# Optimization experiments

Measured on AMD Instinct MI355X. Metric: run time of the kernel, lower is better.

Reference implementation:

```python
import jax, jax.numpy as jnp
import numpy as np

TOP_K = 2          # routed top_k = top_k - num_shared_experts = 3 - 1
CAP_FACTOR = 1.1   # capacity_factor


def setup_inputs() -> dict:
    key = jax.random.key(0)
    ks = jax.random.split(key, 12)
    B, S, D, E = 4, 2048, 1024, 7
    s = 0.02
    return {
        "x": jax.random.normal(ks[0], (B, S, D), jnp.float32),
        "noise": jax.random.normal(ks[1], (B, S, E), jnp.float32),
        "Wr": jax.random.normal(ks[2], (D, E)) * s, "br": jnp.zeros((E,)),
        "Wn": jax.random.normal(ks[3], (D, E)) * s, "bn": jnp.zeros((E,)),
        "W1": jax.random.normal(ks[4], (E, D, D)) * s, "b1": jnp.zeros((E, D)),
        "W2": jax.random.normal(ks[5], (E, D, D)) * s, "b2": jnp.zeros((E, D)),
        "Ws1": jax.random.normal(ks[6], (D, D)) * s, "bs1": jnp.zeros((D,)),
        "Ws2": jax.random.normal(ks[7], (D, D)) * s, "bs2": jnp.zeros((D,)),
    }


def reference(x, noise, Wr, br, Wn, bn, W1, b1, W2, b2, Ws1, bs1, Ws2, bs2):
    B, S, D = x.shape
    E = Wr.shape[1]
    N = B * S
    C = int(N * TOP_K / E * CAP_FACTOR)  # per-expert capacity (static)

    # shared expert (Dropout inactive at inference)
    x_shared = jax.nn.relu(x @ Ws1 + bs1) @ Ws2 + bs2

    # --- noisy top-k router ---
    logits = x @ Wr + br
    noisy = logits + noise * jax.nn.softplus(x @ Wn + bn)
    vals, idx = jax.lax.top_k(noisy, TOP_K)                    # [B,S,K]
    onehot = jax.nn.one_hot(idx, E, dtype=x.dtype)             # [B,S,K,E]
    probs_k = jax.nn.softmax(vals, axis=-1)                    # softmax over -inf-masked logits == softmax over top-k vals
    router_probs = jnp.einsum('bske,bsk->bse', onehot, probs_k)
    expert_mask = onehot.sum(-2)
    lbl = E * (router_probs.mean((0, 1)) * expert_mask.mean((0, 1))).sum()

    # --- capacity-limited dispatch, first-come-first-served in flat token order ---
    flat_x = x.reshape(N, D)
    flat_g = router_probs.reshape(N, E)
    m = (expert_mask.reshape(N, E) > 0).T                      # [E,N] token->expert assignment
    pos = jnp.cumsum(m.astype(jnp.int32), axis=1) - 1          # slot within expert
    valid = m & (pos < C)
    token = jnp.arange(N, dtype=jnp.int32)
    dest = jnp.where(valid, jnp.arange(E, dtype=jnp.int32)[:, None] * C + pos, E * C)
    idxs = jnp.full((E * C + 1,), N, dtype=jnp.int32)
    idxs = idxs.at[dest.reshape(-1)].set(jnp.broadcast_to(token, (E, N)).reshape(-1))
    idxs = idxs[:E * C].reshape(E, C)                          # token id per slot, N = padding

    xpad = jnp.concatenate([flat_x, jnp.zeros((1, D), x.dtype)], axis=0)
    gpad = jnp.concatenate([flat_g, jnp.zeros((1, E), x.dtype)], axis=0)
    xe = xpad[idxs]                                            # [E,C,D]
    h = jax.nn.relu(jnp.einsum('ecd,edh->ech', xe, W1) + b1[:, None, :])
    out = jnp.einsum('ech,ehd->ecd', h, W2) + b2[:, None, :]
    g = (gpad[idxs] * jnp.eye(E, dtype=x.dtype)[:, None, :]).sum(-1)  # [E,C] gate per slot
    slot_valid = (idxs < N).astype(x.dtype)
    weighted = out * (g * slot_valid)[..., None]

    upd = jnp.zeros((N + 1, D), x.dtype).at[idxs.reshape(-1)].add(weighted.reshape(-1, D))[:N]
    final = upd.reshape(B, S, D) + x_shared
    return final, lbl
```

## Files before the change

kernel.cpp:

```cpp
#include <hip/hip_runtime.h>
#include <math.h>

typedef unsigned short u16;
typedef __attribute__((ext_vector_type(4))) float f32x4;
typedef __bf16 bf16x8 __attribute__((ext_vector_type(8)));

#define NTOK 8192
#define DDIM 1024
#define NEXP 7
#define CAPC 2574
#define CPAD 2688
#define EBLK 1176
#define TBLK 1688
#define XCHK 211

__device__ inline float bf2f(u16 u) {
    union { unsigned int i; float f; } c; c.i = ((unsigned int)u) << 16; return c.f;
}
__device__ inline u16 f2bf(float f) {
    union { float f; unsigned int i; } c; c.f = f;
    unsigned int u = c.i;
    unsigned int r = (u + 0x7fffu + ((u >> 16) & 1u)) >> 16;
    return (u16)r;
}

__device__ inline void gl2lds16(const u16* g, const u16* l) {
    __builtin_amdgcn_global_load_lds(
        (const __attribute__((address_space(1))) unsigned int*)g,
        (__attribute__((address_space(3))) unsigned int*)l, 16, 0, 0);
}

__global__ void k_zero(float* out, long n) {
    long i = (long)blockIdx.x * 256 + threadIdx.x;
    long stride = (long)gridDim.x * 256;
    for (; i < n; i += stride) out[i] = 0.f;
}

__device__ inline void tile_transpose(const float* __restrict__ src, u16* __restrict__ dst,
                                      int k0, int n0, int tid, u16 (*tbuf)[256]) {
#pragma unroll
    for (int p = 0; p < 16; ++p) {
        int kl = p * 16 + (tid >> 4);
        int nl = (tid & 15) * 4;
        float4 v = *(const float4*)(src + (long)(k0 + kl) * 1024 + n0 + nl);
        int s = (tid & 7) << 3;
        int kx = kl ^ s;
        tbuf[nl + 0][kx] = f2bf(v.x);
        tbuf[nl + 1][kx] = f2bf(v.y);
        tbuf[nl + 2][kx] = f2bf(v.z);
        tbuf[nl + 3][kx] = f2bf(v.w);
    }
    __syncthreads();
#pragma unroll
    for (int q = 0; q < 8; ++q) {
        int nl = q * 8 + (tid >> 5);
        int kl = (tid & 31) * 8;
        int s = ((nl >> 2) & 7) << 3;
        const u16* pr = &tbuf[nl][kl ^ s];
        ushort4 a = *(const ushort4*)pr;
        ushort4 b = *(const ushort4*)(pr + 4);
        u16* pd = dst + (long)(n0 + nl) * 1024 + k0 + kl;
        *(ushort4*)pd = a;
        *(ushort4*)(pd + 4) = b;
    }
}

__global__ void k_prep(const float* __restrict__ x, u16* __restrict__ xb,
                       int* __restrict__ slot_token, u16* __restrict__ zrow,
                       const float* __restrict__ W1, const float* __restrict__ Ws1,
                       u16* __restrict__ Wt, u16* __restrict__ Wst,
                       const float* __restrict__ W2, const float* __restrict__ Ws2,
                       u16* __restrict__ Wt2, u16* __restrict__ Wst2) {
    __shared__ u16 tbuf[64][256];
    int bid = blockIdx.x, tid = threadIdx.x;
    if (bid < 4096) {
        int gid = bid * 256 + tid;
        int i = gid * 8;
        float4 a = *(const float4*)(x + i);
        float4 b = *(const float4*)(x + i + 4);
        ushort4 o0; o0.x = f2bf(a.x); o0.y = f2bf(a.y); o0.z = f2bf(a.z); o0.w = f2bf(a.w);
        ushort4 o1; o1.x = f2bf(b.x); o1.y = f2bf(b.y); o1.z = f2bf(b.z); o1.w = f2bf(b.w);
        *(ushort4*)(xb + i) = o0;
        *(ushort4*)(xb + i + 4) = o1;
        if (gid < DDIM) zrow[gid] = 0;
        if (gid < NEXP * CPAD) slot_token[gid] = NTOK;
        return;
    }
    int tb = bid - 4096;
    int set = tb >> 9;
    int t9 = tb & 511;
    int z = t9 >> 6;
    int rem = t9 & 63;
    int k0 = (rem >> 4) * 256;
    int n0 = (rem & 15) * 64;
    const float* srcE = set ? W2 : W1;
    const float* srcS = set ? Ws2 : Ws1;
    u16* dE = set ? Wt2 : Wt;
    u16* dS = set ? Wst2 : Wst;
    const float* src; u16* dst;
    if (z < 7) { src = srcE + (long)z * 1048576; dst = dE + (long)z * 1048576; }
    else       { src = srcS;                     dst = dS; }
    tile_transpose(src, dst, k0, n0, tid, tbuf);
}

__global__ void k_transpose(const float* __restrict__ srcE, const float* __restrict__ srcS,
                            u16* __restrict__ Wt, u16* __restrict__ Wst) {
    __shared__ u16 tbuf[64][256];
    int bid = blockIdx.x, tid = threadIdx.x;
    int z = bid >> 6;
    int rem = bid & 63;
    int k0 = (rem >> 4) * 256;
    int n0 = (rem & 15) * 64;
    const float* src; u16* dst;
    if (z < 7) { src = srcE + (long)z * 1048576; dst = Wt + (long)z * 1048576; }
    else       { src = srcS;                     dst = Wst; }
    tile_transpose(src, dst, k0, n0, tid, tbuf);
}

__global__ __launch_bounds__(512) void k_router(
    const float* __restrict__ x,
    const float* __restrict__ Wr, const float* __restrict__ Wn,
    double* __restrict__ arO, double* __restrict__ anO) {
    __shared__ float swr[7168];
    __shared__ float swn[7168];
    int tid = threadIdx.x;
    for (int i = tid; i < 7168; i += 512) { swr[i] = Wr[i]; swn[i] = Wn[i]; }
    __syncthreads();
    int lane = tid & 63, wv = tid >> 6;
    int t = blockIdx.x * 8 + wv;
    double ar[7] = {0,0,0,0,0,0,0}, an[7] = {0,0,0,0,0,0,0};
    for (int j = 0; j < 16; ++j) {
        int d = j * 64 + lane;
        double xd = (double)x[t * 1024 + d];
#pragma unroll
        for (int e = 0; e < 7; ++e) {
            ar[e] += xd * (double)swr[d * 7 + e];
            an[e] += xd * (double)swn[d * 7 + e];
        }
    }
#pragma unroll
    for (int e = 0; e < 7; ++e) {
        for (int o = 32; o > 0; o >>= 1) {
            ar[e] += __shfl_xor(ar[e], o);
            an[e] += __shfl_xor(an[e], o);
        }
    }
    if (lane == 0) {
#pragma unroll
        for (int e = 0; e < 7; ++e) { arO[t * 7 + e] = ar[e]; anO[t * 7 + e] = an[e]; }
    }
}

__global__ void k_tail(const double* __restrict__ arO, const double* __restrict__ anO,
                       const float* __restrict__ noise,
                       const float* __restrict__ br, const float* __restrict__ bn,
                       int* __restrict__ idx0, int* __restrict__ idx1,
                       float* __restrict__ p0, float* __restrict__ p1,
                       int* __restrict__ cntA, double* __restrict__ sumA) {
    int t = blockIdx.x * 256 + threadIdx.x;
    int lane = threadIdx.x & 63;
    double best = -1e300, second = -1e300; int b0 = 0, b1 = 0;
#pragma unroll
    for (int e = 0; e < 7; ++e) {
        double lg = arO[t * 7 + e] + (double)br[e];
        double z  = anO[t * 7 + e] + (double)bn[e];
        double sp = (z > 30.0) ? (z + log1p(exp(-z))) : log1p(exp(z));
        double v  = lg + (double)noise[t * 7 + e] * sp;
        if (v > best)        { second = best; b1 = b0; best = v; b0 = e; }
        else if (v > second) { second = v; b1 = e; }
    }
    double ex = exp(second - best);
    float q0 = (float)(1.0 / (1.0 + ex));
    float q1 = (float)(ex / (1.0 + ex));
    idx0[t] = b0; idx1[t] = b1; p0[t] = q0; p1[t] = q1;
    int chunk = t >> 6;
    double dq0 = (double)q0, dq1 = (double)q1;
#pragma unroll
    for (int e = 0; e < 7; ++e) {
        unsigned long long m = __ballot((b0 == e) || (b1 == e));
        double q = (b0 == e ? dq0 : 0.0) + (b1 == e ? dq1 : 0.0);
        for (int o = 32; o > 0; o >>= 1) q += __shfl_xor(q, o);
        if (lane == 0) { cntA[e * 128 + chunk] = __popcll(m); sumA[e * 128 + chunk] = q; }
    }
}

__global__ void k_scanbase(const int* __restrict__ cntA, const double* __restrict__ sumA,
                           int* __restrict__ baseA, int* __restrict__ cnt,
                           float* __restrict__ out) {
    __shared__ int s[7][128];
    __shared__ double rd[7][128];
    __shared__ int rawc[7];
    __shared__ double ps[7];
    int tid = threadIdx.x;
    int e = tid >> 7, i = tid & 127;
    int v = cntA[e * 128 + i];
    s[e][i] = v;
    rd[e][i] = sumA[e * 128 + i];
    __syncthreads();
    for (int o = 1; o < 128; o <<= 1) {
        int add = (i >= o) ? s[e][i - o] : 0;
        __syncthreads();
        s[e][i] += add;
        __syncthreads();
    }
    baseA[e * 128 + i] = s[e][i] - v;
    if (i == 127) { rawc[e] = s[e][127]; cnt[e] = (s[e][127] < CAPC) ? s[e][127] : CAPC; }
    for (int o = 64; o > 0; o >>= 1) {
        if (i < o) rd[e][i] += rd[e][i + o];
        __syncthreads();
    }
    if (i == 0) ps[e] = rd[e][0];
    __syncthreads();
    if (tid == 0) {
        double acc = 0.0;
        for (int ee = 0; ee < 7; ++ee) acc += ps[ee] * (double)rawc[ee];
        out[(long)NTOK * DDIM] = (float)(7.0 * acc / (8192.0 * 8192.0));
    }
}

__global__ void k_assign(const int* __restrict__ idx0, const int* __restrict__ idx1,
                         const int* __restrict__ baseA, int* __restrict__ slot_token,
                         int* __restrict__ ts0, int* __restrict__ ts1) {
    int lane = threadIdx.x & 63;
    int chunk = (blockIdx.x * 256 + threadIdx.x) >> 6;
    int t = chunk * 64 + lane;
    int i0 = idx0[t], i1 = idx1[t];
    int myts0 = -1, myts1 = -1;
    unsigned long long lt = (1ull << lane) - 1ull;
#pragma unroll
    for (int e = 0; e < 7; ++e) {
        bool has = (i0 == e) || (i1 == e);
        unsigned long long m = __ballot(has);
        int pre = __popcll(m & lt);
        int pos = baseA[e * 128 + chunk] + pre;
        if (has && pos < CAPC) {
            int slot = e * CPAD + pos;
            slot_token[slot] = t;
            if (i0 == e) myts0 = slot; else myts1 = slot;
        }
    }
    ts0[t] = myts0; ts1[t] = myts1;
}

template <bool GATHER, bool MODE_H>
__global__ __launch_bounds__(256) void k_gemm(
    const u16* __restrict__ AbaseE, const u16* __restrict__ AbaseS,
    const int* __restrict__ gidx, const u16* __restrict__ zrow,
    const u16* __restrict__ WtE, const u16* __restrict__ WtS,
    const float* __restrict__ biasE, const float* __restrict__ biasS,
    u16* __restrict__ outE, u16* __restrict__ outS,
    const int* __restrict__ cnt) {
    __shared__ __align__(16) u16 ldsA[128 * 64];
    __shared__ __align__(16) u16 ldsB[128 * 64];
    int phys = blockIdx.x;
    int bid = (phys & 7) * XCHK + (phys >> 3);
    int tid = threadIdx.x, lane = tid & 63, wv = tid >> 6;
    int lrow = lane >> 3, lkg = lane & 7;
    int kgs = lkg ^ lrow;

    int e = 0, my, nx;
    const u16* Ab; const u16* Bb; const float* bias; u16* outp;
    bool gather = false;
    if (bid < EBLK) {
        e = bid / 168; int r = bid % 168; my = r >> 3; nx = r & 7;
        if (my * 128 >= cnt[e]) return;
        Ab = AbaseE + (GATHER ? 0L : (long)e * CPAD * 1024);
        Bb = WtE + ((long)e << 20);
        bias = biasE + e * 1024;
        outp = outE + (long)e * CPAD * 1024;
        gather = GATHER;
    } else {
        int sb = bid - EBLK; my = sb >> 3; nx = sb & 7;
        Ab = AbaseS; Bb = WtS; bias = biasS; outp = outS;
    }
    int m0 = my * 128, n0 = nx * 128;

    const u16* arow[4];
    const u16* brow[4];
#pragma unroll
    for (int i = 0; i < 4; ++i) {
        int r = (wv * 4 + i) * 8 + lrow;
        if (gather) {
            int tok = gidx[e * CPAD + m0 + r];
            arow[i] = (tok < NTOK) ? (AbaseE + (long)tok * DDIM) : zrow;
        } else {
            arow[i] = Ab + (long)(m0 + r) * DDIM;
        }
        brow[i] = Bb + (long)(n0 + r) * DDIM;
    }
    f32x4 acc[4][4];
#pragma unroll
    for (int a = 0; a < 4; ++a)
#pragma unroll
        for (int b = 0; b < 4; ++b) { f32x4 z = {0.f, 0.f, 0.f, 0.f}; acc[a][b] = z; }

    int wm = (wv >> 1) * 64, wn = (wv & 1) * 64;
    int rl = lane & 15, quad = lane >> 4;

    for (int k0 = 0; k0 < 1024; k0 += 64) {
#pragma unroll
        for (int i = 0; i < 4; ++i) {
            gl2lds16(arow[i] + k0 + kgs * 8, &ldsA[(wv * 4 + i) * 512]);
            gl2lds16(brow[i] + k0 + kgs * 8, &ldsB[(wv * 4 + i) * 512]);
        }
        __syncthreads();
#pragma unroll
        for (int ks = 0; ks < 2; ++ks) {
            int kg = ks * 4 + quad;
            bf16x8 af[4], bf[4];
#pragma unroll
            for (int mi = 0; mi < 4; ++mi) {
                int row = wm + mi * 16 + rl;
                af[mi] = *(const bf16x8*)&ldsA[row * 64 + (kg ^ (row & 7)) * 8];
            }
#pragma unroll
            for (int ni = 0; ni < 4; ++ni) {
                int row = wn + ni * 16 + rl;
                bf[ni] = *(const bf16x8*)&ldsB[row * 64 + (kg ^ (row & 7)) * 8];
            }
#pragma unroll
            for (int mi = 0; mi < 4; ++mi)
#pragma unroll
                for (int ni = 0; ni < 4; ++ni)
                    acc[mi][ni] = __builtin_amdgcn_mfma_f32_16x16x32_bf16(
                        af[mi], bf[ni], acc[mi][ni], 0, 0, 0);
        }
        __syncthreads();
    }
#pragma unroll
    for (int ni = 0; ni < 4; ++ni) {
        int col = n0 + wn + ni * 16 + rl;
        float bv = bias[col];
#pragma unroll
        for (int mi = 0; mi < 4; ++mi) {
            int rowb = m0 + wm + mi * 16 + quad * 4;
#pragma unroll
            for (int r = 0; r < 4; ++r) {
                float v = acc[mi][ni][r] + bv;
                if constexpr (MODE_H) v = v > 0.f ? v : 0.f;
                outp[(long)(rowb + r) * DDIM + col] = f2bf(v);
            }
        }
    }
}

__global__ __launch_bounds__(256) void k_combine(
    const u16* __restrict__ Xs, const u16* __restrict__ OutE,
    const int* __restrict__ ts0, const int* __restrict__ ts1,
    const float* __restrict__ p0, const float* __restrict__ p1,
    float* __restrict__ out) {
    int b = blockIdx.x;
    int d = threadIdx.x * 4;
    long base = (long)b * DDIM + d;
    ushort4 xs4 = *(const ushort4*)(Xs + base);
    float r0 = bf2f(xs4.x), r1 = bf2f(xs4.y), r2 = bf2f(xs4.z), r3 = bf2f(xs4.w);
    int s0 = ts0[b], s1 = ts1[b];
    if (s0 >= 0) {
        float g = p0[b];
        ushort4 o4 = *(const ushort4*)(OutE + (long)s0 * DDIM + d);
        r0 += g * bf2f(o4.x); r1 += g * bf2f(o4.y); r2 += g * bf2f(o4.z); r3 += g * bf2f(o4.w);
    }
    if (s1 >= 0) {
        float g = p1[b];
        ushort4 o4 = *(const ushort4*)(OutE + (long)s1 * DDIM + d);
        r0 += g * bf2f(o4.x); r1 += g * bf2f(o4.y); r2 += g * bf2f(o4.z); r3 += g * bf2f(o4.w);
    }
    float4 w; w.x = r0; w.y = r1; w.z = r2; w.w = r3;
    *(float4*)(out + base) = w;
}

extern "C" void kernel_launch(void* const* d_in, const int* in_sizes, int n_in,
                              void* d_out, int out_size, void* d_ws, size_t ws_size,
                              hipStream_t stream) {
    const float* x    = (const float*)d_in[0];
    const float* noise= (const float*)d_in[1];
    const float* Wr   = (const float*)d_in[2];
    const float* br   = (const float*)d_in[3];
    const float* Wn   = (const float*)d_in[4];
    const float* bn   = (const float*)d_in[5];
    const float* W1   = (const float*)d_in[6];
    const float* b1   = (const float*)d_in[7];
    const float* W2   = (const float*)d_in[8];
    const float* b2   = (const float*)d_in[9];
    const float* Ws1  = (const float*)d_in[10];
    const float* bs1  = (const float*)d_in[11];
    const float* Ws2  = (const float*)d_in[12];
    const float* bs2  = (const float*)d_in[13];
    float* out = (float*)d_out;
    char* ws = (char*)d_ws;

    size_t off = 0;
    auto alloc = [&](size_t bytes) { size_t o = off; off += (bytes + 255) & ~(size_t)255; return o; };
    u16*  Wt   = (u16*)(ws + alloc(7ull * 1048576 * 2));
    u16*  Wst  = (u16*)(ws + alloc(1048576ull * 2));
    u16*  xb   = (u16*)(ws + alloc((size_t)NTOK * 1024 * 2));
    u16*  He   = (u16*)(ws + alloc((size_t)NEXP * CPAD * 1024 * 2));
    u16*  Hs   = (u16*)(ws + alloc((size_t)NTOK * 1024 * 2));
    u16*  OutE = (u16*)(ws + alloc((size_t)NEXP * CPAD * 1024 * 2));
    u16*  Xs   = (u16*)(ws + alloc((size_t)NTOK * 1024 * 2));
    int*  idx0 = (int*)(ws + alloc(NTOK * 4));
    int*  idx1 = (int*)(ws + alloc(NTOK * 4));
    float* p0  = (float*)(ws + alloc(NTOK * 4));
    float* p1  = (float*)(ws + alloc(NTOK * 4));
    int*  ts0  = (int*)(ws + alloc(NTOK * 4));
    int*  ts1  = (int*)(ws + alloc(NTOK * 4));
    int*  slot_token = (int*)(ws + alloc(NEXP * CPAD * 4));
    int*  cntA = (int*)(ws + alloc(7 * 128 * 4));
    int*  baseA= (int*)(ws + alloc(7 * 128 * 4));
    double* sumA = (double*)(ws + alloc(7 * 128 * 8));
    int*  cnt    = (int*)(ws + alloc(8 * 4));
    u16*  zrow   = (u16*)(ws + alloc(1024 * 2));
    double* arO  = (double*)(ws + alloc((size_t)NTOK * 7 * 8));
    double* anO  = (double*)(ws + alloc((size_t)NTOK * 7 * 8));
    size_t base_off = off;
    u16*  Wt2  = (u16*)(ws + alloc(7ull * 1048576 * 2));
    u16*  Wst2 = (u16*)(ws + alloc(1048576ull * 2));

    if (base_off > ws_size) {
        k_zero<<<2048, 256, 0, stream>>>(out, (long)out_size);
        return;
    }
    bool sep = (off <= ws_size);
    if (!sep) { Wt2 = Wt; Wst2 = Wst; }

    k_prep<<<sep ? 5120 : 4608, 256, 0, stream>>>(
        x, xb, slot_token, zrow, W1, Ws1, Wt, Wst, W2, Ws2, Wt2, Wst2);
    k_router<<<1024, 512, 0, stream>>>(x, Wr, Wn, arO, anO);
    k_tail<<<32, 256, 0, stream>>>(arO, anO, noise, br, bn, idx0, idx1, p0, p1, cntA, sumA);
    k_scanbase<<<1, 896, 0, stream>>>(cntA, sumA, baseA, cnt, out);
    k_assign<<<32, 256, 0, stream>>>(idx0, idx1, baseA, slot_token, ts0, ts1);

    k_gemm<true, true><<<TBLK, 256, 0, stream>>>(
        xb, xb, slot_token, zrow, Wt, Wst, b1, bs1, He, Hs, cnt);

    if (!sep)
        k_transpose<<<512, 256, 0, stream>>>(W2, Ws2, Wt, Wst);

    k_gemm<false, false><<<TBLK, 256, 0, stream>>>(
        He, Hs, nullptr, zrow, Wt2, Wst2, b2, bs2, OutE, Xs, cnt);

    k_combine<<<NTOK, 256, 0, stream>>>(Xs, OutE, ts0, ts1, p0, p1, out);
    (void)in_sizes; (void)n_in; (void)out_size;
}
```

Baseline: 379.2 us.

## Fuse bf16 conversion and top-k tail into router kernel, rebase scan

The router kernel now also converts x to bf16 and computes softplus, noisy top-2 and gate probabilities inline, so it emits per-block expert counts and sums directly. This removes the separate conversion pass in k_prep, the k_tail launch and the fp64 logit round-trip through global memory. The scan and assign kernels are reworked to use 8-token block granularity, with each scan thread summing 8 entries. Router weights are transposed into an expert-major shared layout to allow float4 reads, which adds a division-based setup loop per block.

```diff
diff --git a/kernel.cpp b/kernel.cpp
--- a/kernel.cpp
+++ b/kernel.cpp
@@ -65,30 +65,21 @@
     }
 }
 
-__global__ void k_prep(const float* __restrict__ x, u16* __restrict__ xb,
-                       int* __restrict__ slot_token, u16* __restrict__ zrow,
+__global__ void k_prep(int* __restrict__ slot_token, u16* __restrict__ zrow,
                        const float* __restrict__ W1, const float* __restrict__ Ws1,
                        u16* __restrict__ Wt, u16* __restrict__ Wst,
                        const float* __restrict__ W2, const float* __restrict__ Ws2,
-                       u16* __restrict__ Wt2, u16* __restrict__ Wst2) {
+                       u16* __restrict__ Wt2, u16* __restrict__ Wst2, int ntb) {
     __shared__ u16 tbuf[64][256];
     int bid = blockIdx.x, tid = threadIdx.x;
-    if (bid < 4096) {
-        int gid = bid * 256 + tid;
-        int i = gid * 8;
-        float4 a = *(const float4*)(x + i);
-        float4 b = *(const float4*)(x + i + 4);
-        ushort4 o0; o0.x = f2bf(a.x); o0.y = f2bf(a.y); o0.z = f2bf(a.z); o0.w = f2bf(a.w);
-        ushort4 o1; o1.x = f2bf(b.x); o1.y = f2bf(b.y); o1.z = f2bf(b.z); o1.w = f2bf(b.w);
-        *(ushort4*)(xb + i) = o0;
-        *(ushort4*)(xb + i + 4) = o1;
+    if (bid >= ntb) {
+        int gid = (bid - ntb) * 256 + tid;
+        if (gid < NEXP * CPAD) slot_token[gid] = NTOK;
         if (gid < DDIM) zrow[gid] = 0;
-        if (gid < NEXP * CPAD) slot_token[gid] = NTOK;
         return;
     }
-    int tb = bid - 4096;
-    int set = tb >> 9;
-    int t9 = tb & 511;
+    int set = bid >> 9;
+    int t9 = bid & 511;
     int z = t9 >> 6;
     int rem = t9 & 63;
     int k0 = (rem >> 4) * 256;
@@ -120,22 +111,40 @@
 __global__ __launch_bounds__(512) void k_router(
     const float* __restrict__ x,
     const float* __restrict__ Wr, const float* __restrict__ Wn,
-    double* __restrict__ arO, double* __restrict__ anO) {
-    __shared__ float swr[7168];
-    __shared__ float swn[7168];
+    const float* __restrict__ br, const float* __restrict__ bn,
+    const float* __restrict__ noise,
+    u16* __restrict__ xb,
+    int* __restrict__ idx0, int* __restrict__ idx1,
+    float* __restrict__ p0, float* __restrict__ p1,
+    int* __restrict__ cnt8, double* __restrict__ sum8) {
+    __shared__ float swr[7][1024];
+    __shared__ float swn[7][1024];
+    __shared__ int sb0[8], sb1[8];
+    __shared__ double sq0[8], sq1[8];
     int tid = threadIdx.x;
-    for (int i = tid; i < 7168; i += 512) { swr[i] = Wr[i]; swn[i] = Wn[i]; }
+    for (int i = tid; i < 7168; i += 512) {
+        int d = i / 7, e = i - d * 7;
+        float vr = Wr[i], vn = Wn[i];
+        swr[e][d] = vr; swn[e][d] = vn;
+    }
     __syncthreads();
     int lane = tid & 63, wv = tid >> 6;
     int t = blockIdx.x * 8 + wv;
     double ar[7] = {0,0,0,0,0,0,0}, an[7] = {0,0,0,0,0,0,0};
-    for (int j = 0; j < 16; ++j) {
-        int d = j * 64 + lane;
-        double xd = (double)x[t * 1024 + d];
+#pragma unroll
+    for (int j = 0; j < 4; ++j) {
+        int d0 = j * 256 + lane * 4;
+        float4 xv = *(const float4*)(x + (long)t * 1024 + d0);
+        ushort4 o; o.x = f2bf(xv.x); o.y = f2bf(xv.y); o.z = f2bf(xv.z); o.w = f2bf(xv.w);
+        *(ushort4*)(xb + (long)t * 1024 + d0) = o;
 #pragma unroll
         for (int e = 0; e < 7; ++e) {
-            ar[e] += xd * (double)swr[d * 7 + e];
-            an[e] += xd * (double)swn[d * 7 + e];
+            float4 w4 = *(const float4*)&swr[e][d0];
+            float4 n4 = *(const float4*)&swn[e][d0];
+            ar[e] += (double)xv.x * (double)w4.x; an[e] += (double)xv.x * (double)n4.x;
+            ar[e] += (double)xv.y * (double)w4.y; an[e] += (double)xv.y * (double)n4.y;
+            ar[e] += (double)xv.z * (double)w4.z; an[e] += (double)xv.z * (double)n4.z;
+            ar[e] += (double)xv.w * (double)w4.w; an[e] += (double)xv.w * (double)n4.w;
         }
     }
 #pragma unroll
@@ -146,46 +155,37 @@
         }
     }
     if (lane == 0) {
-#pragma unroll
-        for (int e = 0; e < 7; ++e) { arO[t * 7 + e] = ar[e]; anO[t * 7 + e] = an[e]; }
-    }
-}
-
-__global__ void k_tail(const double* __restrict__ arO, const double* __restrict__ anO,
-                       const float* __restrict__ noise,
-                       const float* __restrict__ br, const float* __restrict__ bn,
-                       int* __restrict__ idx0, int* __restrict__ idx1,
-                       float* __restrict__ p0, float* __restrict__ p1,
-                       int* __restrict__ cntA, double* __restrict__ sumA) {
-    int t = blockIdx.x * 256 + threadIdx.x;
-    int lane = threadIdx.x & 63;
-    double best = -1e300, second = -1e300; int b0 = 0, b1 = 0;
-#pragma unroll
-    for (int e = 0; e < 7; ++e) {
-        double lg = arO[t * 7 + e] + (double)br[e];
-        double z  = anO[t * 7 + e] + (double)bn[e];
-        double sp = (z > 30.0) ? (z + log1p(exp(-z))) : log1p(exp(z));
-        double v  = lg + (double)noise[t * 7 + e] * sp;
-        if (v > best)        { second = best; b1 = b0; best = v; b0 = e; }
-        else if (v > second) { second = v; b1 = e; }
-    }
-    double ex = exp(second - best);
-    float q0 = (float)(1.0 / (1.0 + ex));
-    float q1 = (float)(ex / (1.0 + ex));
-    idx0[t] = b0; idx1[t] = b1; p0[t] = q0; p1[t] = q1;
-    int chunk = t >> 6;
-    double dq0 = (double)q0, dq1 = (double)q1;
-#pragma unroll
-    for (int e = 0; e < 7; ++e) {
-        unsigned long long m = __ballot((b0 == e) || (b1 == e));
-        double q = (b0 == e ? dq0 : 0.0) + (b1 == e ? dq1 : 0.0);
-        for (int o = 32; o > 0; o >>= 1) q += __shfl_xor(q, o);
-        if (lane == 0) { cntA[e * 128 + chunk] = __popcll(m); sumA[e * 128 + chunk] = q; }
-    }
-}
-
-__global__ void k_scanbase(const int* __restrict__ cntA, const double* __restrict__ sumA,
-                           int* __restrict__ baseA, int* __restrict__ cnt,
+        double best = -1e300, second = -1e300; int b0 = 0, b1 = 0;
+#pragma unroll
+        for (int e = 0; e < 7; ++e) {
+            double lg = ar[e] + (double)br[e];
+            double z  = an[e] + (double)bn[e];
+            double sp = (z > 30.0) ? (z + log1p(exp(-z))) : log1p(exp(z));
+            double v  = lg + (double)noise[t * 7 + e] * sp;
+            if (v > best)        { second = best; b1 = b0; best = v; b0 = e; }
+            else if (v > second) { second = v; b1 = e; }
+        }
+        double ex = exp(second - best);
+        double q0 = 1.0 / (1.0 + ex);
+        double q1 = ex / (1.0 + ex);
+        idx0[t] = b0; idx1[t] = b1; p0[t] = (float)q0; p1[t] = (float)q1;
+        sb0[wv] = b0; sb1[wv] = b1; sq0[wv] = q0; sq1[wv] = q1;
+    }
+    __syncthreads();
+    if (tid < 7) {
+        int c = 0; double s = 0.0;
+#pragma unroll
+        for (int w = 0; w < 8; ++w) {
+            if (sb0[w] == tid) { c++; s += sq0[w]; }
+            if (sb1[w] == tid) { c++; s += sq1[w]; }
+        }
+        cnt8[tid * 1024 + blockIdx.x] = c;
+        sum8[tid * 1024 + blockIdx.x] = s;
+    }
+}
+
+__global__ void k_scanbase(const int* __restrict__ cnt8, const double* __restrict__ sum8,
+                           int* __restrict__ base8, int* __restrict__ cnt,
                            float* __restrict__ out) {
     __shared__ int s[7][128];
     __shared__ double rd[7][128];
@@ -193,9 +193,15 @@
     __shared__ double ps[7];
     int tid = threadIdx.x;
     int e = tid >> 7, i = tid & 127;
-    int v = cntA[e * 128 + i];
+    int c8[8]; int v = 0; double s64 = 0.0;
+#pragma unroll
+    for (int j = 0; j < 8; ++j) {
+        c8[j] = cnt8[e * 1024 + i * 8 + j];
+        v += c8[j];
+        s64 += sum8[e * 1024 + i * 8 + j];
+    }
     s[e][i] = v;
-    rd[e][i] = sumA[e * 128 + i];
+    rd[e][i] = s64;
     __syncthreads();
     for (int o = 1; o < 128; o <<= 1) {
         int add = (i >= o) ? s[e][i - o] : 0;
@@ -203,7 +209,9 @@
         s[e][i] += add;
         __syncthreads();
     }
-    baseA[e * 128 + i] = s[e][i] - v;
+    int run = s[e][i] - v;
+#pragma unroll
+    for (int j = 0; j < 8; ++j) { base8[e * 1024 + i * 8 + j] = run; run += c8[j]; }
     if (i == 127) { rawc[e] = s[e][127]; cnt[e] = (s[e][127] < CAPC) ? s[e][127] : CAPC; }
     for (int o = 64; o > 0; o >>= 1) {
         if (i < o) rd[e][i] += rd[e][i + o];
@@ -219,20 +227,21 @@
 }
 
 __global__ void k_assign(const int* __restrict__ idx0, const int* __restrict__ idx1,
-                         const int* __restrict__ baseA, int* __restrict__ slot_token,
+                         const int* __restrict__ base8, int* __restrict__ slot_token,
                          int* __restrict__ ts0, int* __restrict__ ts1) {
+    int t = blockIdx.x * 256 + threadIdx.x;
     int lane = threadIdx.x & 63;
-    int chunk = (blockIdx.x * 256 + threadIdx.x) >> 6;
-    int t = chunk * 64 + lane;
     int i0 = idx0[t], i1 = idx1[t];
     int myts0 = -1, myts1 = -1;
+    unsigned long long gm = 0xFFull << ((lane >> 3) * 8);
     unsigned long long lt = (1ull << lane) - 1ull;
+    int chunk = t >> 3;
 #pragma unroll
     for (int e = 0; e < 7; ++e) {
         bool has = (i0 == e) || (i1 == e);
         unsigned long long m = __ballot(has);
-        int pre = __popcll(m & lt);
-        int pos = baseA[e * 128 + chunk] + pre;
+        int pre = __popcll(m & lt & gm);
+        int pos = base8[e * 1024 + chunk] + pre;
         if (has && pos < CAPC) {
             int slot = e * CPAD + pos;
             slot_token[slot] = t;
@@ -405,13 +414,11 @@
     int*  ts0  = (int*)(ws + alloc(NTOK * 4));
     int*  ts1  = (int*)(ws + alloc(NTOK * 4));
     int*  slot_token = (int*)(ws + alloc(NEXP * CPAD * 4));
-    int*  cntA = (int*)(ws + alloc(7 * 128 * 4));
-    int*  baseA= (int*)(ws + alloc(7 * 128 * 4));
-    double* sumA = (double*)(ws + alloc(7 * 128 * 8));
+    int*  cnt8  = (int*)(ws + alloc(7 * 1024 * 4));
+    int*  base8 = (int*)(ws + alloc(7 * 1024 * 4));
+    double* sum8 = (double*)(ws + alloc(7 * 1024 * 8));
     int*  cnt    = (int*)(ws + alloc(8 * 4));
     u16*  zrow   = (u16*)(ws + alloc(1024 * 2));
-    double* arO  = (double*)(ws + alloc((size_t)NTOK * 7 * 8));
-    double* anO  = (double*)(ws + alloc((size_t)NTOK * 7 * 8));
     size_t base_off = off;
     u16*  Wt2  = (u16*)(ws + alloc(7ull * 1048576 * 2));
     u16*  Wst2 = (u16*)(ws + alloc(1048576ull * 2));
@@ -422,13 +429,14 @@
     }
     bool sep = (off <= ws_size);
     if (!sep) { Wt2 = Wt; Wst2 = Wst; }
-
-    k_prep<<<sep ? 5120 : 4608, 256, 0, stream>>>(
-        x, xb, slot_token, zrow, W1, Ws1, Wt, Wst, W2, Ws2, Wt2, Wst2);
-    k_router<<<1024, 512, 0, stream>>>(x, Wr, Wn, arO, anO);
-    k_tail<<<32, 256, 0, stream>>>(arO, anO, noise, br, bn, idx0, idx1, p0, p1, cntA, sumA);
-    k_scanbase<<<1, 896, 0, stream>>>(cntA, sumA, baseA, cnt, out);
-    k_assign<<<32, 256, 0, stream>>>(idx0, idx1, baseA, slot_token, ts0, ts1);
+    int ntb = sep ? 1024 : 512;
+
+    k_prep<<<ntb + 74, 256, 0, stream>>>(
+        slot_token, zrow, W1, Ws1, Wt, Wst, W2, Ws2, Wt2, Wst2, ntb);
+    k_router<<<1024, 512, 0, stream>>>(
+        x, Wr, Wn, br, bn, noise, xb, idx0, idx1, p0, p1, cnt8, sum8);
+    k_scanbase<<<1, 896, 0, stream>>>(cnt8, sum8, base8, cnt, out);
+    k_assign<<<32, 256, 0, stream>>>(idx0, idx1, base8, slot_token, ts0, ts1);
 
     k_gemm<true, true><<<TBLK, 256, 0, stream>>>(
         xb, xb, slot_token, zrow, Wt, Wst, b1, bs1, He, Hs, cnt);
```

Result: faster. 371.5 us (-2.0%).
